# Performance work log

Measured on AMD Instinct MI355X. Metric: run time of the kernel, lower is better.

## Reference

```python
import jax, jax.numpy as jnp
import numpy as np

B, F, A, U = 4096, 128, 8, 10  # batch, n_features, num_att, n_outputs
R = 2.0                        # attention amplification factor
BN_EPS = 1e-3                  # keras BatchNormalization default epsilon


def _glorot(key, shape):
    fan_in, fan_out = shape[-2], shape[-1]
    lim = np.sqrt(6.0 / (fan_in + fan_out)).astype(np.float32)
    return jax.random.uniform(key, shape, jnp.float32, -lim, lim)


def setup_inputs() -> dict:
    key = jax.random.key(0)
    k0, k1, k2 = jax.random.split(key, 3)
    x = jax.random.normal(k0, (B, F), jnp.float32)
    # one _Attention per excluded feature j -> stacked kernels [F, A, F, U]
    kernel = _glorot(k1, (F, A, F, U))
    fc_w = _glorot(k2, (A, 1))           # Dense(units=1) over the num_att axis
    fc_b = jnp.zeros((1,), jnp.float32)
    gamma = jnp.ones((1,), jnp.float32)  # BN params (inference / fresh moving stats)
    beta = jnp.zeros((1,), jnp.float32)
    moving_mean = jnp.zeros((1,), jnp.float32)
    moving_var = jnp.ones((1,), jnp.float32)
    return {"x": x, "kernel": kernel, "fc_w": fc_w, "fc_b": fc_b,
            "gamma": gamma, "beta": beta,
            "moving_mean": moving_mean, "moving_var": moving_var}


def reference(x, kernel, fc_w, fc_b, gamma, beta, moving_mean, moving_var):
    nF = x.shape[-1]
    # mask j zeroes out feature j: masks[j, f] = 1 - (j == f)
    masks = 1.0 - jnp.eye(nF, dtype=x.dtype)
    xm = x[None, :, :] * masks[:, None, :]          # [F, B, F] masked inputs
    # per-feature attention: z = softmax(Xm @ K) over units axis
    z = jnp.einsum('jbf,jafu->jabu', xm, kernel)    # [F, A, B, U]
    z = jax.nn.softmax(z, axis=-1)
    w = jnp.exp(kernel * R)                         # [F, A, F, U]
    # attn output per j is z @ w^T -> [F, A, B, F]; fuse the mean over j
    s = jnp.einsum('jabu,jafu->abf', z, w) / nF     # [A, B, F]
    s = jnp.transpose(s, (1, 2, 0))                 # [B, F, A]
    y = s @ fc_w + fc_b                             # [B, F, 1]
    # BatchNormalization in inference mode (moving statistics)
    y = (y - moving_mean) * jax.lax.rsqrt(moving_var + BN_EPS) * gamma + beta
    y = jnp.squeeze(y, -1)                          # [B, F]
    return jax.nn.softmax(y, axis=-1)
```

## Files before the change

### kernel.cpp

```cpp
#include <hip/hip_runtime.h>


#define NJ 8
#define JPC (128 / NJ)

typedef __attribute__((ext_vector_type(8))) short short8v;
typedef __attribute__((ext_vector_type(4))) float f32x4;

__device__ inline unsigned short f2bf(float f) {
    union { float f; unsigned u; } c; c.f = f;
    return (unsigned short)((c.u + 0x7FFFu + ((c.u >> 16) & 1u)) >> 16);
}
__device__ inline float bf2f(unsigned short h) {
    union { unsigned u; float f; } c; c.u = ((unsigned)h) << 16;
    return c.f;
}

__global__ void ife_prep2(const float* __restrict__ K, const float* __restrict__ fc_w,
                          unsigned short* __restrict__ KbT, unsigned short* __restrict__ W2,
                          unsigned short* __restrict__ Kjj) {
    int t = blockIdx.x * 256 + threadIdx.x;
    if (t >= 128 * 8 * 128) return;
    int ja = t >> 7, f = t & 127;
    int j = ja >> 3, a = ja & 7, p = a >> 1, ai = a & 1;
    float wscale = fc_w[a] * (1.0f / 128.0f);
    const float* src = K + (size_t)t * 10;
    unsigned short* w2 = W2 + (((size_t)(j * 4 + p) * 128 + f) * 32) + ai * 16;
#pragma unroll
    for (int u = 0; u < 16; ++u) {
        float kv = (u < 10) ? src[u] : 0.0f;
        unsigned short kb = (u < 10) ? f2bf(kv) : (unsigned short)0;
        KbT[((size_t)ja * 16 + u) * 128 + f] = kb;
        w2[u] = (u < 10) ? f2bf(__expf(2.0f * kv) * wscale) : (unsigned short)0;
        if (f == j) Kjj[ja * 16 + u] = kb;
    }
}

__global__ __launch_bounds__(256, 2) void ife_main2(
    const float* __restrict__ x, const unsigned short* __restrict__ KbT,
    const unsigned short* __restrict__ W2, const unsigned short* __restrict__ Kjj,
    float* __restrict__ yp) {
    __shared__ unsigned xb[64 * 64];
    __shared__ unsigned pb[4 * 64 * 16];

    const int t = threadIdx.x;
    const int btile = blockIdx.x & 63;
    const int chunk = blockIdx.x >> 6;
    const int b0 = btile * 64;
    const int lane = t & 63;
    const int wv = __builtin_amdgcn_readfirstlane(t >> 6);
    const int lr = lane & 15;
    const int lg = lane >> 4;

    for (int i = t; i < 64 * 64; i += 256) {
        int b = i >> 6, dw = i & 63;
        float2 v = *reinterpret_cast<const float2*>(x + (size_t)(b0 + b) * 128 + dw * 2);
        unsigned pk = (unsigned)f2bf(v.x) | ((unsigned)f2bf(v.y) << 16);
        int g = dw >> 2;
        xb[b * 64 + (((g ^ (b & 7)) << 2) | (dw & 3))] = pk;
    }
    __syncthreads();

    short8v xf[16];
#pragma unroll
    for (int ks = 0; ks < 4; ++ks)
#pragma unroll
        for (int nt = 0; nt < 4; ++nt) {
            int b = nt * 16 + lr;
            int g = ks * 4 + lg;
            xf[ks * 4 + nt] = *reinterpret_cast<const short8v*>(
                &xb[b * 64 + ((g ^ (b & 7)) << 2)]);
        }

    f32x4 acc[4][2];
#pragma unroll
    for (int mt = 0; mt < 4; ++mt)
#pragma unroll
        for (int nt = 0; nt < 2; ++nt) acc[mt][nt] = f32x4{0.f, 0.f, 0.f, 0.f};

    const int ub = lg * 4;

#pragma unroll 1
    for (int jj = 0; jj < JPC; ++jj) {
        const int j = chunk * JPC + jj;
#pragma unroll
        for (int ai = 0; ai < 2; ++ai) {
            const int a = wv * 2 + ai;
            const size_t kbase = (size_t)(j * 8 + a) * 16;
            short8v af[4];
#pragma unroll
            for (int ks = 0; ks < 4; ++ks)
                af[ks] = *reinterpret_cast<const short8v*>(
                    KbT + (kbase + lr) * 128 + ks * 32 + lg * 8);
            f32x4 z[4];
#pragma unroll
            for (int nt = 0; nt < 4; ++nt) z[nt] = f32x4{0.f, 0.f, 0.f, 0.f};
#pragma unroll
            for (int ks = 0; ks < 4; ++ks)
#pragma unroll
                for (int nt = 0; nt < 4; ++nt)
                    z[nt] = __builtin_amdgcn_mfma_f32_16x16x32_bf16(
                        af[ks], xf[ks * 4 + nt], z[nt], 0, 0, 0);
            unsigned short kj0, kj1, kj2, kj3;
            {
                const unsigned short* kp = Kjj + kbase + ub;
                kj0 = kp[0]; kj1 = kp[1]; kj2 = kp[2]; kj3 = kp[3];
            }
            const int gj = j >> 3;
#pragma unroll
            for (int nt = 0; nt < 4; ++nt) {
                int b = nt * 16 + lr;
                unsigned pkx = xb[b * 64 + (((gj ^ (b & 7)) << 2) | ((j >> 1) & 3))];
                float xbj = bf2f((unsigned short)((j & 1) ? (pkx >> 16) : (pkx & 0xFFFFu)));
                z[nt][0] = fmaf(-bf2f(kj0), xbj, z[nt][0]);
                z[nt][1] = fmaf(-bf2f(kj1), xbj, z[nt][1]);
                z[nt][2] = fmaf(-bf2f(kj2), xbj, z[nt][2]);
                z[nt][3] = fmaf(-bf2f(kj3), xbj, z[nt][3]);
            }
#pragma unroll
            for (int nt = 0; nt < 4; ++nt) {
                float m = -3.0e38f;
#pragma unroll
                for (int q = 0; q < 4; ++q)
                    m = (ub + q < 10) ? fmaxf(m, z[nt][q]) : m;
                m = fmaxf(m, __shfl_xor(m, 16, 64));
                m = fmaxf(m, __shfl_xor(m, 32, 64));
                float e0 = (ub + 0 < 10) ? __expf(z[nt][0] - m) : 0.f;
                float e1 = (ub + 1 < 10) ? __expf(z[nt][1] - m) : 0.f;
                float e2 = (ub + 2 < 10) ? __expf(z[nt][2] - m) : 0.f;
                float e3 = (ub + 3 < 10) ? __expf(z[nt][3] - m) : 0.f;
                float s = e0 + e1 + e2 + e3;
                s += __shfl_xor(s, 16, 64);
                s += __shfl_xor(s, 32, 64);
                float inv = 1.0f / s;
                int b = nt * 16 + lr;
                unsigned pk0 = (unsigned)f2bf(e0 * inv) | ((unsigned)f2bf(e1 * inv) << 16);
                unsigned pk1 = (unsigned)f2bf(e2 * inv) | ((unsigned)f2bf(e3 * inv) << 16);
                int dw0 = ai * 8 + lg * 2;
                int base = (wv * 64 + b) * 16;
                int swz = (b >> 1) & 3;
                pb[base + ((((dw0 >> 2) ^ swz) << 2) | (dw0 & 3))] = pk0;
                pb[base + ((((dw0 + 1) >> 2) ^ swz) << 2) + ((dw0 + 1) & 3)] = pk1;
            }
        }
        __syncthreads();
#pragma unroll
        for (int p = 0; p < 4; ++p) {
            short8v wf[2];
#pragma unroll
            for (int nt = 0; nt < 2; ++nt) {
                int f = wv * 32 + nt * 16 + lr;
                wf[nt] = *reinterpret_cast<const short8v*>(
                    W2 + (((size_t)(j * 4 + p) * 128 + f) * 32) + lg * 8);
            }
#pragma unroll
            for (int mt = 0; mt < 4; ++mt) {
                int b = mt * 16 + lr;
                short8v pf = *reinterpret_cast<const short8v*>(
                    &pb[(p * 64 + b) * 16 + ((lg ^ ((b >> 1) & 3)) << 2)]);
#pragma unroll
                for (int nt = 0; nt < 2; ++nt)
                    acc[mt][nt] = __builtin_amdgcn_mfma_f32_16x16x32_bf16(
                        pf, wf[nt], acc[mt][nt], 0, 0, 0);
            }
        }
        __syncthreads();
    }
    float* ypb = yp + ((size_t)chunk * 4096 + b0) * 128;
#pragma unroll
    for (int mt = 0; mt < 4; ++mt)
#pragma unroll
        for (int nt = 0; nt < 2; ++nt) {
            int f = wv * 32 + nt * 16 + lr;
#pragma unroll
            for (int q = 0; q < 4; ++q) {
                int b = mt * 16 + lg * 4 + q;
                ypb[(size_t)b * 128 + f] = acc[mt][nt][q];
            }
        }
}

__global__ void ife_final(const float* __restrict__ yp, const float* __restrict__ fc_b,
                          const float* __restrict__ gamma, const float* __restrict__ beta,
                          const float* __restrict__ mmean, const float* __restrict__ mvar,
                          float* __restrict__ out) {
    const int b = blockIdx.x;
    const int f = threadIdx.x;
    float s = 0.f;
#pragma unroll
    for (int n = 0; n < NJ; ++n)
        s += yp[((size_t)n * 4096 + b) * 128 + f];
    const float scale = gamma[0] * rsqrtf(mvar[0] + 1e-3f);
    float y = (s + fc_b[0] - mmean[0]) * scale + beta[0];

    __shared__ float redm[2], reds[2];
    float m = y;
#pragma unroll
    for (int o = 32; o >= 1; o >>= 1) m = fmaxf(m, __shfl_xor(m, o, 64));
    const int wid = f >> 6;
    if ((f & 63) == 0) redm[wid] = m;
    __syncthreads();
    m = fmaxf(redm[0], redm[1]);
    float e = __expf(y - m);
    float ss = e;
#pragma unroll
    for (int o = 32; o >= 1; o >>= 1) ss += __shfl_xor(ss, o, 64);
    if ((f & 63) == 0) reds[wid] = ss;
    __syncthreads();
    out[(size_t)b * 128 + f] = e / (reds[0] + reds[1]);
}

extern "C" void kernel_launch(void* const* d_in, const int* in_sizes, int n_in,
                              void* d_out, int out_size, void* d_ws, size_t ws_size,
                              hipStream_t stream) {
    const float* x     = (const float*)d_in[0];
    const float* K     = (const float*)d_in[1];
    const float* fc_w  = (const float*)d_in[2];
    const float* fc_b  = (const float*)d_in[3];
    const float* gamma = (const float*)d_in[4];
    const float* beta  = (const float*)d_in[5];
    const float* mmean = (const float*)d_in[6];
    const float* mvar  = (const float*)d_in[7];
    float* out = (float*)d_out;

    unsigned short* KbT = (unsigned short*)d_ws;
    unsigned short* W2  = KbT + 2097152;
    unsigned short* Kjj = W2 + 2097152;
    float* yp = (float*)((char*)d_ws + 8421376);

    hipLaunchKernelGGL(ife_prep2, dim3(512),     dim3(256), 0, stream, K, fc_w, KbT, W2, Kjj);
    hipLaunchKernelGGL(ife_main2, dim3(64 * NJ), dim3(256), 0, stream, x, KbT, W2, Kjj, yp);
    hipLaunchKernelGGL(ife_final, dim3(4096),    dim3(128), 0, stream,
                       yp, fc_b, gamma, beta, mmean, mvar, out);
}
```

Measured before the change: 179.2 us.

## Coalesce prep writes via LDS staging and split j over more chunks

The prep kernel now stages the bf16 kernel and exp-weight tables in shared memory, so global writes are coalesced 32-bit stores instead of strided 16-bit scatters. The main kernel takes the j-chunk count at runtime and uses 16 chunks when the workspace is large enough, doubling the grid to 1024 blocks, and launch bounds now target 4 blocks per CU for more occupancy. The cost is a larger partial-sum buffer and twice the reads in the final reduction kernel.

```diff
diff --git a/kernel.cpp b/kernel.cpp
--- a/kernel.cpp
+++ b/kernel.cpp
@@ -1,8 +1,5 @@
 #include <hip/hip_runtime.h>
 
-
-#define NJ 8
-#define JPC (128 / NJ)
 
 typedef __attribute__((ext_vector_type(8))) short short8v;
 typedef __attribute__((ext_vector_type(4))) float f32x4;
@@ -16,30 +13,53 @@
     return c.f;
 }
 
-__global__ void ife_prep2(const float* __restrict__ K, const float* __restrict__ fc_w,
-                          unsigned short* __restrict__ KbT, unsigned short* __restrict__ W2,
-                          unsigned short* __restrict__ Kjj) {
-    int t = blockIdx.x * 256 + threadIdx.x;
-    if (t >= 128 * 8 * 128) return;
-    int ja = t >> 7, f = t & 127;
-    int j = ja >> 3, a = ja & 7, p = a >> 1, ai = a & 1;
-    float wscale = fc_w[a] * (1.0f / 128.0f);
-    const float* src = K + (size_t)t * 10;
-    unsigned short* w2 = W2 + (((size_t)(j * 4 + p) * 128 + f) * 32) + ai * 16;
+__global__ __launch_bounds__(256) void ife_prep3(
+    const float* __restrict__ K, const float* __restrict__ fc_w,
+    unsigned short* __restrict__ KbT, unsigned short* __restrict__ W2,
+    unsigned short* __restrict__ Kjj) {
+    const int j = blockIdx.x >> 2, p = blockIdx.x & 3;
+    const int t = threadIdx.x;
+    __shared__ unsigned short wt[128 * 32];
+    __shared__ unsigned short kt[2 * 128 * 16];
+    const int ai = t >> 7, f = t & 127, a = p * 2 + ai;
+    const float* src = K + (size_t)((j * 8 + a) * 128 + f) * 10;
+    const float wscale = fc_w[a] * (1.0f / 128.0f);
+    float kv[10];
+#pragma unroll
+    for (int u = 0; u < 10; ++u) kv[u] = src[u];
 #pragma unroll
     for (int u = 0; u < 16; ++u) {
-        float kv = (u < 10) ? src[u] : 0.0f;
-        unsigned short kb = (u < 10) ? f2bf(kv) : (unsigned short)0;
-        KbT[((size_t)ja * 16 + u) * 128 + f] = kb;
-        w2[u] = (u < 10) ? f2bf(__expf(2.0f * kv) * wscale) : (unsigned short)0;
-        if (f == j) Kjj[ja * 16 + u] = kb;
-    }
-}
-
-__global__ __launch_bounds__(256, 2) void ife_main2(
+        unsigned short kb = (u < 10) ? f2bf(kv[u]) : (unsigned short)0;
+        kt[(ai * 128 + f) * 16 + u] = kb;
+        wt[f * 32 + ai * 16 + u] =
+            (u < 10) ? f2bf(__expf(2.0f * kv[u]) * wscale) : (unsigned short)0;
+        if (f == j) Kjj[(size_t)(j * 8 + a) * 16 + u] = kb;
+    }
+    __syncthreads();
+    {
+        const unsigned* s = (const unsigned*)wt;
+        unsigned* d = (unsigned*)(W2 + (size_t)(j * 4 + p) * 128 * 32);
+#pragma unroll
+        for (int i = 0; i < 8; ++i) d[i * 256 + t] = s[i * 256 + t];
+    }
+#pragma unroll
+    for (int a2 = 0; a2 < 2; ++a2) {
+        unsigned* d = (unsigned*)(KbT + (size_t)((j * 8 + p * 2 + a2) * 16) * 128);
+#pragma unroll
+        for (int i = 0; i < 4; ++i) {
+            int dd = i * 256 + t;
+            int u = dd >> 6, f2 = (dd & 63) * 2;
+            unsigned lo = kt[(a2 * 128 + f2) * 16 + u];
+            unsigned hi = kt[(a2 * 128 + f2 + 1) * 16 + u];
+            d[dd] = lo | (hi << 16);
+        }
+    }
+}
+
+__global__ __launch_bounds__(256, 4) void ife_main2(
     const float* __restrict__ x, const unsigned short* __restrict__ KbT,
     const unsigned short* __restrict__ W2, const unsigned short* __restrict__ Kjj,
-    float* __restrict__ yp) {
+    float* __restrict__ yp, int jpc) {
     __shared__ unsigned xb[64 * 64];
     __shared__ unsigned pb[4 * 64 * 16];
 
@@ -81,8 +101,8 @@
     const int ub = lg * 4;
 
 #pragma unroll 1
-    for (int jj = 0; jj < JPC; ++jj) {
-        const int j = chunk * JPC + jj;
+    for (int jj = 0; jj < jpc; ++jj) {
+        const int j = chunk * jpc + jj;
 #pragma unroll
         for (int ai = 0; ai < 2; ++ai) {
             const int a = wv * 2 + ai;
@@ -183,12 +203,12 @@
 __global__ void ife_final(const float* __restrict__ yp, const float* __restrict__ fc_b,
                           const float* __restrict__ gamma, const float* __restrict__ beta,
                           const float* __restrict__ mmean, const float* __restrict__ mvar,
-                          float* __restrict__ out) {
+                          float* __restrict__ out, int nj) {
     const int b = blockIdx.x;
     const int f = threadIdx.x;
     float s = 0.f;
-#pragma unroll
-    for (int n = 0; n < NJ; ++n)
+#pragma unroll 1
+    for (int n = 0; n < nj; ++n)
         s += yp[((size_t)n * 4096 + b) * 128 + f];
     const float scale = gamma[0] * rsqrtf(mvar[0] + 1e-3f);
     float y = (s + fc_b[0] - mmean[0]) * scale + beta[0];
@@ -226,10 +246,14 @@
     unsigned short* KbT = (unsigned short*)d_ws;
     unsigned short* W2  = KbT + 2097152;
     unsigned short* Kjj = W2 + 2097152;
-    float* yp = (float*)((char*)d_ws + 8421376);
-
-    hipLaunchKernelGGL(ife_prep2, dim3(512),     dim3(256), 0, stream, K, fc_w, KbT, W2, Kjj);
-    hipLaunchKernelGGL(ife_main2, dim3(64 * NJ), dim3(256), 0, stream, x, KbT, W2, Kjj, yp);
+    const size_t tab_bytes = 8421376;
+    float* yp = (float*)((char*)d_ws + tab_bytes);
+
+    int nj = (ws_size >= tab_bytes + (size_t)16 * 4096 * 128 * 4) ? 16 : 8;
+    int jpc = 128 / nj;
+
+    hipLaunchKernelGGL(ife_prep3, dim3(512),     dim3(256), 0, stream, K, fc_w, KbT, W2, Kjj);
+    hipLaunchKernelGGL(ife_main2, dim3(64 * nj), dim3(256), 0, stream, x, KbT, W2, Kjj, yp, jpc);
     hipLaunchKernelGGL(ife_final, dim3(4096),    dim3(128), 0, stream,
-                       yp, fc_b, gamma, beta, mmean, mvar, out);
-}
+                       yp, fc_b, gamma, beta, mmean, mvar, out, nj);
+}
```

Result: slower. 226.4 us (+26.4%).
